# Optimization experiments

Hardware: AMD Instinct MI355X
Metric: run time of the kernel (lower is better)

Reference implementation:

```python
import jax, jax.numpy as jnp
import numpy as np

E, K, D, H, C = 32768, 32, 128, 4, 10
DH = D // H

def setup_inputs() -> dict:
    key = jax.random.key(0)
    ks = jax.random.split(key, 9)
    s = 1.0 / np.sqrt(D)
    return {
        "edge_feats": jax.random.normal(ks[0], (E, D), jnp.float32),
        "Wq": jax.random.normal(ks[1], (D, D), jnp.float32) * s,
        "Wk": jax.random.normal(ks[2], (D, D), jnp.float32) * s,
        "Wv": jax.random.normal(ks[3], (D, D), jnp.float32) * s,
        "Wo": jax.random.normal(ks[4], (D, D), jnp.float32) * s,
        "W1": jax.random.normal(ks[5], (D, D), jnp.float32) * s,
        "b1": jnp.zeros((D,), jnp.float32),
        "W2": jax.random.normal(ks[6], (D, C), jnp.float32) * s,
        "b2": jnp.zeros((C,), jnp.float32),
        "edge_adj": jax.random.randint(ks[7], (E, K), 0, E, jnp.int32),
    }

def reference(edge_feats, Wq, Wk, Wv, Wo, W1, b1, W2, b2, edge_adj):
    # Edge attention: each edge attends over its K adjacent edges.
    q = (edge_feats @ Wq).reshape(E, H, DH)                 # [E,H,dh]
    k_all = edge_feats @ Wk                                  # [E,D]
    v_all = edge_feats @ Wv                                  # [E,D]
    kn = k_all[edge_adj].reshape(E, K, H, DH)                # gather [E,K,H,dh]
    vn = v_all[edge_adj].reshape(E, K, H, DH)                # gather [E,K,H,dh]
    scores = jnp.einsum("ehd,ekhd->ehk", q, kn) / np.sqrt(DH)
    attn = jax.nn.softmax(scores, axis=-1)                   # [E,H,K]
    ctx = jnp.einsum("ehk,ekhd->ehd", attn, vn).reshape(E, D)
    edge_out = ctx @ Wo                                       # [E,D]
    # classifier: Linear -> GELU -> Linear
    h = jax.nn.gelu(edge_out @ W1 + b1)
    logits = h @ W2 + b2                                      # [E,C]
    return logits
```

## Files before the change

### kernel.cpp

```cpp
#include <hip/hip_runtime.h>
#include <hip/hip_bf16.h>

constexpr int E_EDGES = 32768;
constexpr int DIM = 128;

using bf16x8 = __attribute__((ext_vector_type(8))) short;
using f32x4  = __attribute__((ext_vector_type(4))) float;

__device__ inline float bflo(unsigned u) { return __uint_as_float(u << 16); }
__device__ inline float bfhi(unsigned u) { return __uint_as_float(u & 0xffff0000u); }
__device__ inline unsigned pk_bf2(float a, float b) {
    __hip_bfloat162 h = __float22bfloat162_rn(make_float2(a, b));
    return *(unsigned*)&h;
}

__global__ __launch_bounds__(256) void k_prep(
    const float* __restrict__ Wq, const float* __restrict__ Wk,
    const float* __restrict__ Wv, const float* __restrict__ Wo,
    const float* __restrict__ W1, __hip_bfloat16* __restrict__ Wt,
    __hip_bfloat16* __restrict__ wft) {
    const int b = blockIdx.x;
    const int t = threadIdx.x;
    if (b < 3) {
        const float* W = (b == 0) ? Wq : (b == 1) ? Wk : Wv;
        __hip_bfloat16* dst = Wt + b * 16384;
#pragma unroll
        for (int i = 0; i < 8; ++i) {
            int idx = i * 2048 + t * 8;
            int k = idx >> 7, n0 = idx & 127;
            float4 f0 = *(const float4*)(W + k * 128 + n0);
            float4 f1 = *(const float4*)(W + k * 128 + n0 + 4);
            float f[8] = {f0.x, f0.y, f0.z, f0.w, f1.x, f1.y, f1.z, f1.w};
#pragma unroll
            for (int j = 0; j < 8; ++j)
                dst[(n0 + j) * 128 + k] = __float2bfloat16(f[j]);
        }
    } else {
        int idx = (b - 3) * 256 + t;
        int r = idx >> 7, c = idx & 127;
        float acc = 0.f;
#pragma unroll 16
        for (int k = 0; k < 128; ++k)
            acc = fmaf(Wo[r * 128 + k], W1[k * 128 + c], acc);
        wft[c * 128 + r] = __float2bfloat16(acc);
    }
}

__global__ __launch_bounds__(256) void k_qkv(
    const float* __restrict__ feats, const __hip_bfloat16* __restrict__ Wt,
    float* __restrict__ qo, __hip_bfloat16* __restrict__ ko,
    __hip_bfloat16* __restrict__ vo) {
    __shared__ short Als[16384];
    __shared__ short Bls[16384];

    const int t = threadIdx.x;
    const int lane = t & 63;
    const int w = t >> 6;
    const int wm = w >> 1, wn = w & 1;
    const int row0 = blockIdx.x * 128;

#pragma unroll
    for (int i = 0; i < 8; ++i) {
        int idx = i * 2048 + t * 8;
        int r = idx >> 7, k0 = idx & 127;
        float4 f0 = *(const float4*)(feats + (size_t)(row0 + r) * DIM + k0);
        float4 f1 = *(const float4*)(feats + (size_t)(row0 + r) * DIM + k0 + 4);
        uint4 o = make_uint4(pk_bf2(f0.x, f0.y), pk_bf2(f0.z, f0.w),
                             pk_bf2(f1.x, f1.y), pk_bf2(f1.z, f1.w));
        *(uint4*)&Als[(r * 128 + k0) ^ ((r & 7) << 3)] = o;
    }
#pragma unroll
    for (int i = 0; i < 8; ++i) {
        int idx = i * 2048 + t * 8;
        int n = idx >> 7, k0 = idx & 127;
        uint4 v = *(const uint4*)(Wt + n * 128 + k0);
        *(uint4*)&Bls[(n * 128 + k0) ^ ((n & 7) << 3)] = v;
    }
    __syncthreads();

    bf16x8 afr[4][4];
#pragma unroll
    for (int m = 0; m < 4; ++m)
#pragma unroll
        for (int ks = 0; ks < 4; ++ks) {
            int r = wm * 64 + m * 16 + (lane & 15);
            int kb = ks * 32 + (lane >> 4) * 8;
            afr[m][ks] = *(bf16x8*)&Als[(r * 128 + kb) ^ ((r & 7) << 3)];
        }

    for (int proj = 0; proj < 3; ++proj) {
        f32x4 acc[4][4];
#pragma unroll
        for (int m = 0; m < 4; ++m)
#pragma unroll
            for (int n = 0; n < 4; ++n) acc[m][n] = (f32x4){0.f, 0.f, 0.f, 0.f};

#pragma unroll
        for (int ks = 0; ks < 4; ++ks) {
            bf16x8 bfr[4];
#pragma unroll
            for (int n = 0; n < 4; ++n) {
                int nn = wn * 64 + n * 16 + (lane & 15);
                int kb = ks * 32 + (lane >> 4) * 8;
                bfr[n] = *(bf16x8*)&Bls[(nn * 128 + kb) ^ ((nn & 7) << 3)];
            }
#pragma unroll
            for (int m = 0; m < 4; ++m)
#pragma unroll
                for (int n = 0; n < 4; ++n)
                    acc[m][n] = __builtin_amdgcn_mfma_f32_16x16x32_bf16(
                        afr[m][ks], bfr[n], acc[m][n], 0, 0, 0);
        }

        if (proj == 0) {
#pragma unroll
            for (int m = 0; m < 4; ++m) {
                int rb = row0 + wm * 64 + m * 16 + (lane >> 4) * 4;
#pragma unroll
                for (int n = 0; n < 4; ++n) {
                    int c = wn * 64 + n * 16 + (lane & 15);
#pragma unroll
                    for (int r = 0; r < 4; ++r)
                        qo[(size_t)(rb + r) * DIM + c] = acc[m][n][r];
                }
            }
        } else {
            __hip_bfloat16* dst = (proj == 1) ? ko : vo;
#pragma unroll
            for (int n = 0; n < 4; ++n) {
                int c = wn * 64 + n * 16 + (lane & 15);
                int h = c >> 5, pr = h & 1;
                int slot = ((h >> 1) << 5) + (c & 31);
                size_t base = (size_t)pr * E_EDGES * 64 + slot;
#pragma unroll
                for (int m = 0; m < 4; ++m) {
                    int rb = row0 + wm * 64 + m * 16 + (lane >> 4) * 4;
#pragma unroll
                    for (int r = 0; r < 4; ++r)
                        dst[base + (size_t)(rb + r) * 64] =
                            __float2bfloat16(acc[m][n][r]);
                }
            }
        }

        if (proj < 2) {
            __syncthreads();
#pragma unroll
            for (int i = 0; i < 8; ++i) {
                int idx = i * 2048 + t * 8;
                int n = idx >> 7, k0 = idx & 127;
                uint4 v = *(const uint4*)(Wt + (proj + 1) * 16384 + n * 128 + k0);
                *(uint4*)&Bls[(n * 128 + k0) ^ ((n & 7) << 3)] = v;
            }
            __syncthreads();
        }
    }
}

__global__ __launch_bounds__(256) void k_attn_pass(
    const float* __restrict__ qc, const __hip_bfloat16* __restrict__ kp,
    const __hip_bfloat16* __restrict__ vp, const int* __restrict__ adj,
    __hip_bfloat16* __restrict__ ctxb, int pass) {
    __shared__ float attn_s[4][64];
    __shared__ int adj_s[4][32];

    const int lane = threadIdx.x & 63;
    const int wid = threadIdx.x >> 6;
    const int e = blockIdx.x * 4 + wid;
    const int n = lane & 31;
    const int g = lane >> 5;

    if (lane < 32) adj_s[wid][lane] = adj[e * 32 + lane];

    const float4* q4 = (const float4*)(qc + (size_t)e * DIM + (pass + 2 * g) * 32);
    float qa[32];
#pragma unroll
    for (int j = 0; j < 8; ++j) {
        float4 tA = q4[j];
        qa[j * 4 + 0] = tA.x; qa[j * 4 + 1] = tA.y;
        qa[j * 4 + 2] = tA.z; qa[j * 4 + 3] = tA.w;
    }

    const int row = adj_s[wid][n];
    const uint4* kr = (const uint4*)(kp + ((size_t)pass * E_EDGES + row) * 64 + g * 32);
    float s0 = 0.f;
#pragma unroll
    for (int j = 0; j < 4; ++j) {
        uint4 u = kr[j];
        s0 = fmaf(qa[j * 8 + 0], bflo(u.x), s0); s0 = fmaf(qa[j * 8 + 1], bfhi(u.x), s0);
        s0 = fmaf(qa[j * 8 + 2], bflo(u.y), s0); s0 = fmaf(qa[j * 8 + 3], bfhi(u.y), s0);
        s0 = fmaf(qa[j * 8 + 4], bflo(u.z), s0); s0 = fmaf(qa[j * 8 + 5], bfhi(u.z), s0);
        s0 = fmaf(qa[j * 8 + 6], bflo(u.w), s0); s0 = fmaf(qa[j * 8 + 7], bfhi(u.w), s0);
    }
    s0 *= 0.17677669529663689f;

    float m0 = s0;
#pragma unroll
    for (int off = 16; off; off >>= 1) m0 = fmaxf(m0, __shfl_xor(m0, off));
    float e0 = __expf(s0 - m0);
    float sum0 = e0;
#pragma unroll
    for (int off = 16; off; off >>= 1) sum0 += __shfl_xor(sum0, off);
    attn_s[wid][g * 32 + n] = e0 / sum0;

    const int d4 = lane & 15;
    const int grp = lane >> 4;
    const int gi = d4 >> 3;
    float4 c = make_float4(0.f, 0.f, 0.f, 0.f);
#pragma unroll
    for (int i = 0; i < 8; ++i) {
        int nn = grp * 8 + i;
        int r2 = adj_s[wid][nn];
        float a = attn_s[wid][gi * 32 + nn];
        uint2 u = *(const uint2*)(vp + ((size_t)pass * E_EDGES + r2) * 64 + d4 * 4);
        c.x = fmaf(a, bflo(u.x), c.x); c.y = fmaf(a, bfhi(u.x), c.y);
        c.z = fmaf(a, bflo(u.y), c.z); c.w = fmaf(a, bfhi(u.y), c.w);
    }
    c.x += __shfl_xor(c.x, 16); c.y += __shfl_xor(c.y, 16);
    c.z += __shfl_xor(c.z, 16); c.w += __shfl_xor(c.w, 16);
    c.x += __shfl_xor(c.x, 32); c.y += __shfl_xor(c.y, 32);
    c.z += __shfl_xor(c.z, 32); c.w += __shfl_xor(c.w, 32);
    if (lane < 16) {
        int h2 = pass + 2 * gi;
        uint2 o;
        o.x = pk_bf2(c.x, c.y);
        o.y = pk_bf2(c.z, c.w);
        *(uint2*)(ctxb + (size_t)e * DIM + h2 * 32 + (d4 & 7) * 4) = o;
    }
}

__global__ __launch_bounds__(256) void k_mlp(
    const __hip_bfloat16* __restrict__ ctxb, const __hip_bfloat16* __restrict__ wft,
    const float* __restrict__ b1, const float* __restrict__ W2,
    const float* __restrict__ b2, float* __restrict__ out) {
    __shared__ short Als[16384];
    __shared__ short Bls[16384];
    __shared__ float w2s[1280];
    __shared__ float b1s[128];
    __shared__ float b2s[16];

    const int t = threadIdx.x;
    const int lane = t & 63;
    const int w = t >> 6;
    const int wm = w >> 1, wn = w & 1;
    const int row0 = blockIdx.x * 128;

#pragma unroll
    for (int i = 0; i < 8; ++i) {
        int idx = i * 2048 + t * 8;
        int r = idx >> 7, k0 = idx & 127;
        uint4 v = *(const uint4*)(ctxb + (size_t)(row0 + r) * DIM + k0);
        *(uint4*)&Als[(r * 128 + k0) ^ ((r & 7) << 3)] = v;
    }
#pragma unroll
    for (int i = 0; i < 8; ++i) {
        int idx = i * 2048 + t * 8;
        int n = idx >> 7, k0 = idx & 127;
        uint4 v = *(const uint4*)(wft + n * 128 + k0);
        *(uint4*)&Bls[(n * 128 + k0) ^ ((n & 7) << 3)] = v;
    }
    for (int i = t; i < 1280; i += 256) w2s[i] = W2[i];
    if (t < 128) b1s[t] = b1[t];
    if (t < 10) b2s[t] = b2[t];
    __syncthreads();

    f32x4 acc[4][4];
#pragma unroll
    for (int m = 0; m < 4; ++m)
#pragma unroll
        for (int n = 0; n < 4; ++n) acc[m][n] = (f32x4){0.f, 0.f, 0.f, 0.f};

#pragma unroll
    for (int ks = 0; ks < 4; ++ks) {
        bf16x8 afr[4], bfr[4];
#pragma unroll
        for (int m = 0; m < 4; ++m) {
            int r = wm * 64 + m * 16 + (lane & 15);
            int kb = ks * 32 + (lane >> 4) * 8;
            afr[m] = *(bf16x8*)&Als[(r * 128 + kb) ^ ((r & 7) << 3)];
        }
#pragma unroll
        for (int n = 0; n < 4; ++n) {
            int nn = wn * 64 + n * 16 + (lane & 15);
            int kb = ks * 32 + (lane >> 4) * 8;
            bfr[n] = *(bf16x8*)&Bls[(nn * 128 + kb) ^ ((nn & 7) << 3)];
        }
#pragma unroll
        for (int m = 0; m < 4; ++m)
#pragma unroll
            for (int n = 0; n < 4; ++n)
                acc[m][n] = __builtin_amdgcn_mfma_f32_16x16x32_bf16(
                    afr[m], bfr[n], acc[m][n], 0, 0, 0);
    }

    __syncthreads();
#pragma unroll
    for (int m = 0; m < 4; ++m) {
        int lr0 = wm * 64 + m * 16 + (lane >> 4) * 4;
#pragma unroll
        for (int n = 0; n < 4; ++n) {
            int c = wn * 64 + n * 16 + (lane & 15);
            float bc = b1s[c];
#pragma unroll
            for (int r = 0; r < 4; ++r) {
                float x = acc[m][n][r] + bc;
                float u = 0.7978845608028654f * (x + 0.044715f * x * x * x);
                float ex = __expf(2.f * u);
                float th = 1.f - 2.f / (ex + 1.f);
                float h = 0.5f * x * (1.f + th);
                int lr = lr0 + r;
                Als[(lr * 128 + c) ^ ((lr & 7) << 3)] =
                    (short)(__bfloat16_as_ushort(__float2bfloat16(h)));
            }
        }
    }
    __syncthreads();

    {
        int r = t >> 1;
        int c0 = (t & 1) * 5;
        float a0 = b2s[c0], a1 = b2s[c0 + 1], a2 = b2s[c0 + 2],
              a3 = b2s[c0 + 3], a4 = b2s[c0 + 4];
#pragma unroll 8
        for (int kk = 0; kk < 128; ++kk) {
            float hv = __uint_as_float(
                ((unsigned)(unsigned short)Als[(r * 128 + kk) ^ ((r & 7) << 3)]) << 16);
            const float* wrow = &w2s[kk * 10 + c0];
            a0 = fmaf(hv, wrow[0], a0);
            a1 = fmaf(hv, wrow[1], a1);
            a2 = fmaf(hv, wrow[2], a2);
            a3 = fmaf(hv, wrow[3], a3);
            a4 = fmaf(hv, wrow[4], a4);
        }
        float* o = out + (size_t)(row0 + r) * 10 + c0;
        o[0] = a0; o[1] = a1; o[2] = a2; o[3] = a3; o[4] = a4;
    }
}

extern "C" void kernel_launch(void* const* d_in, const int* in_sizes, int n_in,
                              void* d_out, int out_size, void* d_ws, size_t ws_size,
                              hipStream_t stream) {
    const float* feats = (const float*)d_in[0];
    const float* Wq    = (const float*)d_in[1];
    const float* Wk    = (const float*)d_in[2];
    const float* Wv    = (const float*)d_in[3];
    const float* Wo    = (const float*)d_in[4];
    const float* W1    = (const float*)d_in[5];
    const float* b1    = (const float*)d_in[6];
    const float* W2    = (const float*)d_in[7];
    const float* b2    = (const float*)d_in[8];
    const int*   adj   = (const int*)d_in[9];
    float* out = (float*)d_out;

    float* ws = (float*)d_ws;
    const size_t ED = (size_t)E_EDGES * DIM;
    float* qbuf = ws;
    __hip_bfloat16* kbuf = (__hip_bfloat16*)(ws + ED);
    __hip_bfloat16* vbuf = kbuf + ED;
    __hip_bfloat16* ctxb = vbuf + ED;
    __hip_bfloat16* wt   = ctxb + ED;
    __hip_bfloat16* wft  = wt + 3 * 16384;

    k_prep<<<67, 256, 0, stream>>>(Wq, Wk, Wv, Wo, W1, wt, wft);
    k_qkv<<<E_EDGES / 128, 256, 0, stream>>>(feats, wt, qbuf, kbuf, vbuf);
    k_attn_pass<<<E_EDGES / 4, 256, 0, stream>>>(qbuf, kbuf, vbuf, adj, ctxb, 0);
    k_attn_pass<<<E_EDGES / 4, 256, 0, stream>>>(qbuf, kbuf, vbuf, adj, ctxb, 1);
    k_mlp<<<E_EDGES / 128, 256, 0, stream>>>(ctxb, wft, b1, W2, b2, out);
}
```

Before: 110.9 us.

## Split attention into score and PV kernels with bf16 Q and weights

```diff
diff --git a/kernel.cpp b/kernel.cpp
--- a/kernel.cpp
+++ b/kernel.cpp
@@ -6,6 +6,8 @@
 
 using bf16x8 = __attribute__((ext_vector_type(8))) short;
 using f32x4  = __attribute__((ext_vector_type(4))) float;
+typedef unsigned int uint4v __attribute__((ext_vector_type(4)));
+typedef unsigned int uint2v __attribute__((ext_vector_type(2)));
 
 __device__ inline float bflo(unsigned u) { return __uint_as_float(u << 16); }
 __device__ inline float bfhi(unsigned u) { return __uint_as_float(u & 0xffff0000u); }
@@ -48,8 +50,8 @@
 
 __global__ __launch_bounds__(256) void k_qkv(
     const float* __restrict__ feats, const __hip_bfloat16* __restrict__ Wt,
-    float* __restrict__ qo, __hip_bfloat16* __restrict__ ko,
-    __hip_bfloat16* __restrict__ vo) {
+    __hip_bfloat16* __restrict__ qp, __hip_bfloat16* __restrict__ kp,
+    __hip_bfloat16* __restrict__ vp) {
     __shared__ short Als[16384];
     __shared__ short Bls[16384];
 
@@ -112,20 +114,8 @@
                         afr[m][ks], bfr[n], acc[m][n], 0, 0, 0);
         }
 
-        if (proj == 0) {
-#pragma unroll
-            for (int m = 0; m < 4; ++m) {
-                int rb = row0 + wm * 64 + m * 16 + (lane >> 4) * 4;
-#pragma unroll
-                for (int n = 0; n < 4; ++n) {
-                    int c = wn * 64 + n * 16 + (lane & 15);
-#pragma unroll
-                    for (int r = 0; r < 4; ++r)
-                        qo[(size_t)(rb + r) * DIM + c] = acc[m][n][r];
-                }
-            }
-        } else {
-            __hip_bfloat16* dst = (proj == 1) ? ko : vo;
+        {
+            __hip_bfloat16* dst = (proj == 0) ? qp : (proj == 1) ? kp : vp;
 #pragma unroll
             for (int n = 0; n < 4; ++n) {
                 int c = wn * 64 + n * 16 + (lane & 15);
@@ -157,11 +147,9 @@
     }
 }
 
-__global__ __launch_bounds__(256) void k_attn_pass(
-    const float* __restrict__ qc, const __hip_bfloat16* __restrict__ kp,
-    const __hip_bfloat16* __restrict__ vp, const int* __restrict__ adj,
-    __hip_bfloat16* __restrict__ ctxb, int pass) {
-    __shared__ float attn_s[4][64];
+__global__ __launch_bounds__(256) void k_score(
+    const __hip_bfloat16* __restrict__ qp, const __hip_bfloat16* __restrict__ kp,
+    const int* __restrict__ adj, unsigned short* __restrict__ aw, int pass) {
     __shared__ int adj_s[4][32];
 
     const int lane = threadIdx.x & 63;
@@ -170,19 +158,24 @@
     const int n = lane & 31;
     const int g = lane >> 5;
 
-    if (lane < 32) adj_s[wid][lane] = adj[e * 32 + lane];
-
-    const float4* q4 = (const float4*)(qc + (size_t)e * DIM + (pass + 2 * g) * 32);
+    if (lane < 32)
+        adj_s[wid][lane] = __builtin_nontemporal_load(adj + e * 32 + lane);
+
+    const uint4v* qr =
+        (const uint4v*)(qp + ((size_t)pass * E_EDGES + e) * 64 + g * 32);
     float qa[32];
 #pragma unroll
-    for (int j = 0; j < 8; ++j) {
-        float4 tA = q4[j];
-        qa[j * 4 + 0] = tA.x; qa[j * 4 + 1] = tA.y;
-        qa[j * 4 + 2] = tA.z; qa[j * 4 + 3] = tA.w;
+    for (int j = 0; j < 4; ++j) {
+        uint4v u = __builtin_nontemporal_load(qr + j);
+        qa[j * 8 + 0] = bflo(u[0]); qa[j * 8 + 1] = bfhi(u[0]);
+        qa[j * 8 + 2] = bflo(u[1]); qa[j * 8 + 3] = bfhi(u[1]);
+        qa[j * 8 + 4] = bflo(u[2]); qa[j * 8 + 5] = bfhi(u[2]);
+        qa[j * 8 + 6] = bflo(u[3]); qa[j * 8 + 7] = bfhi(u[3]);
     }
 
     const int row = adj_s[wid][n];
-    const uint4* kr = (const uint4*)(kp + ((size_t)pass * E_EDGES + row) * 64 + g * 32);
+    const uint4* kr =
+        (const uint4*)(kp + ((size_t)pass * E_EDGES + row) * 64 + g * 32);
     float s0 = 0.f;
 #pragma unroll
     for (int j = 0; j < 4; ++j) {
@@ -201,7 +194,30 @@
     float sum0 = e0;
 #pragma unroll
     for (int off = 16; off; off >>= 1) sum0 += __shfl_xor(sum0, off);
-    attn_s[wid][g * 32 + n] = e0 / sum0;
+    float wgt = e0 / sum0;
+
+    __builtin_nontemporal_store(
+        __bfloat16_as_ushort(__float2bfloat16(wgt)),
+        aw + ((size_t)pass * E_EDGES + e) * 64 + g * 32 + n);
+}
+
+__global__ __launch_bounds__(256) void k_pv(
+    const __hip_bfloat16* __restrict__ vp, const unsigned short* __restrict__ aw,
+    const int* __restrict__ adj, __hip_bfloat16* __restrict__ ctxb, int pass) {
+    __shared__ unsigned short aws[4][64];
+    __shared__ int adj_s[4][32];
+
+    const int lane = threadIdx.x & 63;
+    const int wid = threadIdx.x >> 6;
+    const int e = blockIdx.x * 4 + wid;
+
+    if (lane < 32)
+        adj_s[wid][lane] = __builtin_nontemporal_load(adj + e * 32 + lane);
+    if (lane < 16) {
+        uint2v a2 = __builtin_nontemporal_load(
+            (const uint2v*)(aw + ((size_t)pass * E_EDGES + e) * 64) + lane);
+        *(uint2v*)&aws[wid][lane * 4] = a2;
+    }
 
     const int d4 = lane & 15;
     const int grp = lane >> 4;
@@ -211,7 +227,7 @@
     for (int i = 0; i < 8; ++i) {
         int nn = grp * 8 + i;
         int r2 = adj_s[wid][nn];
-        float a = attn_s[wid][gi * 32 + nn];
+        float a = __uint_as_float((unsigned)aws[wid][gi * 32 + nn] << 16);
         uint2 u = *(const uint2*)(vp + ((size_t)pass * E_EDGES + r2) * 64 + d4 * 4);
         c.x = fmaf(a, bflo(u.x), c.x); c.y = fmaf(a, bfhi(u.x), c.y);
         c.z = fmaf(a, bflo(u.y), c.z); c.w = fmaf(a, bfhi(u.y), c.w);
@@ -222,10 +238,11 @@
     c.z += __shfl_xor(c.z, 32); c.w += __shfl_xor(c.w, 32);
     if (lane < 16) {
         int h2 = pass + 2 * gi;
-        uint2 o;
-        o.x = pk_bf2(c.x, c.y);
-        o.y = pk_bf2(c.z, c.w);
-        *(uint2*)(ctxb + (size_t)e * DIM + h2 * 32 + (d4 & 7) * 4) = o;
+        uint2v o;
+        o[0] = pk_bf2(c.x, c.y);
+        o[1] = pk_bf2(c.z, c.w);
+        __builtin_nontemporal_store(
+            o, (uint2v*)(ctxb + (size_t)e * DIM + h2 * 32 + (d4 & 7) * 4));
     }
 }
 
@@ -352,18 +369,21 @@
     const int*   adj   = (const int*)d_in[9];
     float* out = (float*)d_out;
 
-    float* ws = (float*)d_ws;
-    const size_t ED = (size_t)E_EDGES * DIM;
-    float* qbuf = ws;
-    __hip_bfloat16* kbuf = (__hip_bfloat16*)(ws + ED);
-    __hip_bfloat16* vbuf = kbuf + ED;
-    __hip_bfloat16* ctxb = vbuf + ED;
-    __hip_bfloat16* wt   = ctxb + ED;
+    const size_t ED2 = (size_t)E_EDGES * 64;
+    __hip_bfloat16* base = (__hip_bfloat16*)d_ws;
+    __hip_bfloat16* qp   = base;
+    __hip_bfloat16* kp   = qp + 2 * ED2;
+    __hip_bfloat16* vp   = kp + 2 * ED2;
+    __hip_bfloat16* ctxb = vp + 2 * ED2;
+    unsigned short* aw   = (unsigned short*)(ctxb + 2 * ED2);
+    __hip_bfloat16* wt   = (__hip_bfloat16*)(aw + 2 * ED2);
     __hip_bfloat16* wft  = wt + 3 * 16384;
 
     k_prep<<<67, 256, 0, stream>>>(Wq, Wk, Wv, Wo, W1, wt, wft);
-    k_qkv<<<E_EDGES / 128, 256, 0, stream>>>(feats, wt, qbuf, kbuf, vbuf);
-    k_attn_pass<<<E_EDGES / 4, 256, 0, stream>>>(qbuf, kbuf, vbuf, adj, ctxb, 0);
-    k_attn_pass<<<E_EDGES / 4, 256, 0, stream>>>(qbuf, kbuf, vbuf, adj, ctxb, 1);
+    k_qkv<<<E_EDGES / 128, 256, 0, stream>>>(feats, wt, qp, kp, vp);
+    k_score<<<E_EDGES / 4, 256, 0, stream>>>(qp, kp, adj, aw, 0);
+    k_score<<<E_EDGES / 4, 256, 0, stream>>>(qp, kp, adj, aw, 1);
+    k_pv<<<E_EDGES / 4, 256, 0, stream>>>(vp, aw, adj, ctxb, 0);
+    k_pv<<<E_EDGES / 4, 256, 0, stream>>>(vp, aw, adj, ctxb, 1);
     k_mlp<<<E_EDGES / 128, 256, 0, stream>>>(ctxb, wft, b1, W2, b2, out);
 }
```

New measurement: 119.0 us. +7.3%, slower.
